# Kernel optimization log

Hardware: AMD Instinct MI355X
Metric: run time of the kernel (lower is better)

The kernel has to match this reference:

```python
import math
import jax, jax.numpy as jnp
import numpy as np

B, S, E, H = 2, 2048, 1024, 16
Dh = E // H  # 64
ROPE_BASE = 10000.0


def setup_inputs() -> dict:
    key = jax.random.key(0)
    ks = jax.random.split(key, 7)
    f32 = jnp.float32
    return {
        "q": jax.random.normal(ks[0], (B, S, E), dtype=f32),
        "k": jax.random.normal(ks[1], (B, S, E), dtype=f32),
        "v": jax.random.normal(ks[2], (B, S, E), dtype=f32),
        # nn.Linear weights stored torch-style as [out_features, in_features]
        "W_q": jax.random.normal(ks[3], (E, E), dtype=f32) * 0.02,
        "W_k": jax.random.normal(ks[4], (E, E), dtype=f32) * 0.02,
        "W_v": jax.random.normal(ks[5], (E, E), dtype=f32) * 0.02,
        "W_o": jax.random.normal(ks[6], (E, E), dtype=f32) * 0.02,
    }


def _rope(x):
    # x: [B, H, S, Dh]; interleaved-pair rotary embedding along the seq axis.
    d = x.shape[-1]
    pos = jnp.arange(x.shape[2], dtype=x.dtype)
    inv_freq = 1.0 / (ROPE_BASE ** (jnp.arange(0, d, 2, dtype=x.dtype) / d))
    ang = pos[:, None] * inv_freq            # [S, Dh//2]
    cos, sin = jnp.cos(ang), jnp.sin(ang)    # broadcast over [B, H]
    xe, xo = x[..., 0::2], x[..., 1::2]      # even/odd interleaved pairs
    out = jnp.stack([xe * cos - xo * sin, xo * cos + xe * sin], axis=-1)
    return out.reshape(x.shape)


def reference(q, k, v, W_q, W_k, W_v, W_o):
    b, s, e = q.shape
    scale = 1.0 / math.sqrt(e)  # NOTE: 1/sqrt(hidden_dim), not head_dim (faithful)
    # project and split heads: [B, H, S, Dh]
    qh = (q @ W_q.T).reshape(b, s, H, Dh).transpose(0, 2, 1, 3)
    kh = (k @ W_k.T).reshape(b, s, H, Dh).transpose(0, 2, 1, 3)
    vh = (v @ W_v.T).reshape(b, s, H, Dh).transpose(0, 2, 1, 3)
    qh = _rope(qh)
    kh = _rope(kh)
    scores = jnp.einsum('bhsd,bhtd->bhst', qh, kh) * scale
    # Faithful quirk: the original sets causal_mask[0,0] = False, which zeroes
    # the ENTIRE [S,S] mask (dims 0,1 are singletons) -> masked_fill is a no-op.
    probs = jax.nn.softmax(scores, axis=-1)
    out = jnp.einsum('bhst,bhtd->bhsd', probs, vh)
    out = out.transpose(0, 2, 1, 3).reshape(b, s, e)
    return out @ W_o.T
```

## Files before the change

kernel.cpp:

```cpp
#include <hip/hip_runtime.h>
#include <math.h>

#define Bsz 2
#define Ssz 2048
#define Esz 1024
#define Hn  16
#define Dd  64
#define PADC 72
#define TP   136
#define FP   68

typedef unsigned short ushort_t;
typedef short bf16x8 __attribute__((ext_vector_type(8)));
typedef short bf16x4 __attribute__((ext_vector_type(4)));
typedef float f32x4 __attribute__((ext_vector_type(4)));

#define GLD16(g, l) __builtin_amdgcn_global_load_lds(                        \
    (const __attribute__((address_space(1))) unsigned int*)(g),              \
    (__attribute__((address_space(3))) unsigned int*)(l), 16, 0, 0)

#define KF 0.045084220027780106f

#define MFMA32(a, b, c) __builtin_amdgcn_mfma_f32_16x16x32_bf16((a), (b), (c), 0, 0, 0)
#define MFMA16(a, b, c) __builtin_amdgcn_mfma_f32_16x16x16bf16_1k((a), (b), (c), 0, 0, 0)

__device__ inline ushort_t bf16_rn(float x)
{
    unsigned u = __float_as_uint(x);
    return (ushort_t)((u + 0x7FFFu + ((u >> 16) & 1u)) >> 16);
}

__global__ __launch_bounds__(256) void cvt_kernel(
    const float* s0, const float* s1, const float* s2, const float* s3,
    const float* s4, const float* s5, const float* s6,
    ushort_t* d0, ushort_t* d1, ushort_t* d2, ushort_t* d3,
    ushort_t* d4, ushort_t* d5, ushort_t* d6,
    float* tc, float* ts, int n_big, int n_small)
{
    if (blockIdx.z == 7) {
        const int idx = blockIdx.x * 256 + threadIdx.x;
        if (idx < Ssz * 32) {
            const int s = idx >> 5, p = idx & 31;
            const double c = 9.210340371976184257 / 32.0;
            const double inv = exp(-c * (double)p);
            double sn, cs;
            sincos((double)s * inv, &sn, &cs);
            tc[idx] = (float)cs;
            ts[idx] = (float)sn;
        }
        return;
    }
    const float* s; ushort_t* d;
    switch (blockIdx.z) {
        case 0: s = s0; d = d0; break;
        case 1: s = s1; d = d1; break;
        case 2: s = s2; d = d2; break;
        case 3: s = s3; d = d3; break;
        case 4: s = s4; d = d4; break;
        case 5: s = s5; d = d5; break;
        default: s = s6; d = d6; break;
    }
    const int n = (blockIdx.z < 3) ? n_big : n_small;
    const int i = (blockIdx.x * 256 + threadIdx.x) * 4;
    if (i >= n) return;
    float4 v = *(const float4*)(s + i);
    ushort4 o;
    o.x = bf16_rn(v.x); o.y = bf16_rn(v.y);
    o.z = bf16_rn(v.z); o.w = bf16_rn(v.w);
    *(ushort4*)(d + i) = o;
}

__global__ __launch_bounds__(256) void proj_gemm_kernel(
    const ushort_t* __restrict__ Aq, const ushort_t* __restrict__ Ak,
    const ushort_t* __restrict__ Av,
    const ushort_t* __restrict__ Wq, const ushort_t* __restrict__ Wk,
    const ushort_t* __restrict__ Wv,
    ushort_t* __restrict__ Yq, ushort_t* __restrict__ Yk,
    ushort_t* __restrict__ Yv,
    const float* __restrict__ tc, const float* __restrict__ ts)
{
    const int z = blockIdx.z;
    const ushort_t* Ag = (z == 0) ? Aq : (z == 1) ? Ak : Av;
    const ushort_t* Wg = (z == 0) ? Wq : (z == 1) ? Wk : Wv;
    ushort_t*       Yg = (z == 0) ? Yq : (z == 1) ? Yk : Yv;

    __shared__ __align__(16) char smem[128 * TP * 2];
    ushort_t* sA = (ushort_t*)smem;
    ushort_t* sB = sA + 128 * 32;
    ushort_t* Tb = (ushort_t*)smem;

    const int t    = threadIdx.x;
    const int lane = t & 63;
    const int w    = t >> 6;
    const int wm   = (w & 1) * 64;
    const int wn   = (w >> 1) * 64;
    const int fr   = lane & 15;
    const int g    = lane >> 4;
    const int kq   = g * 8;
    const int n0   = blockIdx.x * 128;
    const int m0   = blockIdx.y * 128;

    const ushort_t* pA = Ag + (size_t)(m0 + (t >> 2)) * 1024 + (t & 3) * 8;
    const ushort_t* pB = Wg + (size_t)(n0 + (t >> 2)) * 1024 + (t & 3) * 8;

    f32x4 acc[4][4];
#pragma unroll
    for (int mi = 0; mi < 4; ++mi)
#pragma unroll
        for (int ni = 0; ni < 4; ++ni) acc[mi][ni] = (f32x4)0.f;

    for (int k0 = 0; k0 < 1024; k0 += 32) {
        GLD16(pA + k0,             &sA[t * 8]);
        GLD16(pA + k0 + 64 * 1024, &sA[2048 + t * 8]);
        GLD16(pB + k0,             &sB[t * 8]);
        GLD16(pB + k0 + 64 * 1024, &sB[2048 + t * 8]);
        __syncthreads();

        bf16x8 a[4], b[4];
#pragma unroll
        for (int mi = 0; mi < 4; ++mi)
            a[mi] = *(const bf16x8*)&sA[(wm + mi * 16 + fr) * 32 + kq];
#pragma unroll
        for (int ni = 0; ni < 4; ++ni)
            b[ni] = *(const bf16x8*)&sB[(wn + ni * 16 + fr) * 32 + kq];
#pragma unroll
        for (int mi = 0; mi < 4; ++mi)
#pragma unroll
            for (int ni = 0; ni < 4; ++ni)
                acc[mi][ni] = MFMA32(a[mi], b[ni], acc[mi][ni]);
        __syncthreads();
    }

#pragma unroll
    for (int mi = 0; mi < 4; ++mi)
#pragma unroll
        for (int ni = 0; ni < 4; ++ni) {
            const int col = wn + ni * 16 + fr;
            const int d   = (n0 + col) & 63;
            const int pi  = d >> 1;
#pragma unroll
            for (int rg = 0; rg < 4; ++rg) {
                const int row = wm + mi * 16 + g * 4 + rg;
                const int s   = (m0 + row) & (Ssz - 1);
                float v  = acc[mi][ni][rg];
                float pt = __shfl_xor(v, 1, 64);
                float o  = v;
                if (z < 2) {
                    const float cs = tc[s * 32 + pi];
                    const float sn = ts[s * 32 + pi];
                    o = (d & 1) ? fmaf(v, cs, pt * sn)
                                : fmaf(v, cs, -pt * sn);
                    if (z == 0) o *= KF;
                }
                Tb[row * TP + col] = bf16_rn(o);
            }
        }
    __syncthreads();

    if (z < 2) {
        const int row = t >> 1;
        const int m   = m0 + row;
        const int b   = m >> 11, s = m & (Ssz - 1);
#pragma unroll
        for (int i = 0; i < 8; ++i) {
            const int ic = (t & 1) * 8 + i;
            uint4 val = *(const uint4*)&Tb[row * TP + ic * 8];
            const int hh = (n0 >> 6) + (ic >> 3);
            const int d  = (ic & 7) * 8;
            *(uint4*)&Yg[(((size_t)(b * Hn + hh)) * Ssz + s) * Dd + d] = val;
        }
    } else {
        const int col = t >> 1;
        const int hh  = (n0 >> 6) + (col >> 6);
        const int d   = col & 63;
        const int b   = m0 >> 11;
        const int sg  = (m0 & (Ssz - 1)) + (t & 1) * 64;
        const size_t base = (((size_t)(b * Hn + hh)) * Dd + d) * Ssz + sg;
#pragma unroll
        for (int jj = 0; jj < 8; ++jj) {
            uint4 val;
            unsigned vv[4];
#pragma unroll
            for (int qd = 0; qd < 4; ++qd) {
                const int r0 = (t & 1) * 64 + jj * 8 + qd * 2;
                const unsigned lo = Tb[(r0 + 0) * TP + col];
                const unsigned hi = Tb[(r0 + 1) * TP + col];
                vv[qd] = lo | (hi << 16);
            }
            val.x = vv[0]; val.y = vv[1]; val.z = vv[2]; val.w = vv[3];
            *(uint4*)&Yg[base + jj * 8] = val;
        }
    }
}

__global__ __launch_bounds__(256) void attn_kernel(
    const ushort_t* __restrict__ Qb, const ushort_t* __restrict__ Kb,
    const ushort_t* __restrict__ Vtb, ushort_t* __restrict__ Ob)
{
    __shared__ __align__(16) ushort_t sKV[4][64 * PADC];

    const int t    = threadIdx.x;
    const int lane = t & 63;
    const int w    = t >> 6;
    const int fr   = lane & 15;
    const int g    = lane >> 4;
    const int kq   = g * 8;
    const int bh   = blockIdx.y;
    const int q0   = blockIdx.x * 128;

    bf16x8 qa[2][2];
#pragma unroll
    for (int mt = 0; mt < 2; ++mt) {
        const size_t qbase = ((size_t)bh * Ssz + q0 + w * 32 + mt * 16 + fr) * Dd;
        qa[mt][0] = *(const bf16x8*)(Qb + qbase + kq);
        qa[mt][1] = *(const bf16x8*)(Qb + qbase + 32 + kq);
    }

    float lp[2] = {0.f, 0.f};
    f32x4 Oacc[2][4];
#pragma unroll
    for (int mt = 0; mt < 2; ++mt)
#pragma unroll
        for (int dt = 0; dt < 4; ++dt) Oacc[mt][dt] = (f32x4)0.f;

    const int srow = t >> 3;
    const int scol = (t & 7) * 8;
    const size_t kgb = (size_t)bh * Ssz * Dd;
    const size_t vgb = (size_t)bh * Dd * Ssz;

#pragma unroll
    for (int rr = 0; rr < 2; ++rr) {
        const int row = srow + rr * 32;
        *(uint4*)&sKV[0][row * PADC + scol] =
            *(const uint4*)(Kb + kgb + (size_t)row * Dd + scol);
        *(uint4*)&sKV[2][row * PADC + scol] =
            *(const uint4*)(Vtb + vgb + (size_t)row * Ssz + scol);
    }
    __syncthreads();

    int cur = 0;
    for (int kv0 = 0; kv0 < Ssz; kv0 += 64) {
        const bool more = (kv0 + 64 < Ssz);
        uint4 nk[2], nv[2];
        if (more) {
#pragma unroll
            for (int rr = 0; rr < 2; ++rr) {
                const int row = srow + rr * 32;
                nk[rr] = *(const uint4*)(Kb + kgb + (size_t)(kv0 + 64 + row) * Dd + scol);
                nv[rr] = *(const uint4*)(Vtb + vgb + (size_t)row * Ssz + kv0 + 64 + scol);
            }
        }
        const ushort_t* sK = sKV[cur];
        const ushort_t* sV = sKV[2 + cur];

        f32x4 St[2][4];
#pragma unroll
        for (int mt = 0; mt < 2; ++mt)
#pragma unroll
            for (int nt = 0; nt < 4; ++nt) St[mt][nt] = (f32x4)0.f;
#pragma unroll
        for (int ks = 0; ks < 2; ++ks)
#pragma unroll
            for (int nt = 0; nt < 4; ++nt) {
                bf16x8 kfrag = *(const bf16x8*)&sK[(nt * 16 + fr) * PADC + ks * 32 + kq];
#pragma unroll
                for (int mt = 0; mt < 2; ++mt)
                    St[mt][nt] = MFMA32(kfrag, qa[mt][ks], St[mt][nt]);
            }

        bf16x4 pf[2][4];
#pragma unroll
        for (int mt = 0; mt < 2; ++mt)
#pragma unroll
            for (int nt = 0; nt < 4; ++nt) {
                const float p0 = exp2f(St[mt][nt][0]);
                const float p1 = exp2f(St[mt][nt][1]);
                const float p2 = exp2f(St[mt][nt][2]);
                const float p3 = exp2f(St[mt][nt][3]);
                lp[mt] += (p0 + p1) + (p2 + p3);
                union { unsigned u[2]; bf16x4 s; } pk;
                pk.u[0] = (__float_as_uint(p0) >> 16) | (__float_as_uint(p1) & 0xFFFF0000u);
                pk.u[1] = (__float_as_uint(p2) >> 16) | (__float_as_uint(p3) & 0xFFFF0000u);
                pf[mt][nt] = pk.s;
            }

#pragma unroll
        for (int nt = 0; nt < 4; ++nt)
#pragma unroll
            for (int dt = 0; dt < 4; ++dt) {
                bf16x4 vfrag = *(const bf16x4*)&sV[(dt * 16 + fr) * PADC + nt * 16 + g * 4];
#pragma unroll
                for (int mt = 0; mt < 2; ++mt)
                    Oacc[mt][dt] = MFMA16(pf[mt][nt], vfrag, Oacc[mt][dt]);
            }

        if (more) {
#pragma unroll
            for (int rr = 0; rr < 2; ++rr) {
                const int row = srow + rr * 32;
                *(uint4*)&sKV[cur ^ 1][row * PADC + scol] = nk[rr];
                *(uint4*)&sKV[2 + (cur ^ 1)][row * PADC + scol] = nv[rr];
            }
            __syncthreads();
            cur ^= 1;
        }
    }

#pragma unroll
    for (int mt = 0; mt < 2; ++mt) {
        lp[mt] += __shfl_xor(lp[mt], 16, 64);
        lp[mt] += __shfl_xor(lp[mt], 32, 64);
    }

    const int b = bh >> 4, h = bh & 15;
#pragma unroll
    for (int mt = 0; mt < 2; ++mt)
#pragma unroll
        for (int rg = 0; rg < 4; ++rg) {
            const float lv  = __shfl(lp[mt], (lane & 48) + g * 4 + rg, 64);
            const float inv = 1.f / lv;
            const int s = q0 + w * 32 + mt * 16 + g * 4 + rg;
#pragma unroll
            for (int dt = 0; dt < 4; ++dt) {
                const float o = Oacc[mt][dt][rg] * inv;
                Ob[((size_t)(b * Ssz + s)) * Esz + h * Dd + dt * 16 + fr] = bf16_rn(o);
            }
        }
}

__global__ __launch_bounds__(256) void final_gemm_kernel(
    const ushort_t* __restrict__ Ag, const ushort_t* __restrict__ Bg,
    float* __restrict__ Yf)
{
    __shared__ __align__(16) char smem[128 * FP * 4];
    ushort_t* sA = (ushort_t*)smem;
    ushort_t* sB = sA + 128 * 32;
    float*    Tf = (float*)smem;

    const int t    = threadIdx.x;
    const int lane = t & 63;
    const int w    = t >> 6;
    const int wm   = (w & 1) * 64;
    const int wn   = (w >> 1) * 32;
    const int fr   = lane & 15;
    const int g    = lane >> 4;
    const int kq   = g * 8;
    const int n0   = blockIdx.x * 64;
    const int m0   = blockIdx.y * 128;

    const ushort_t* pA = Ag + (size_t)(m0 + (t >> 2)) * 1024 + (t & 3) * 8;
    const ushort_t* pB = Bg + (size_t)(n0 + (t >> 2)) * 1024 + (t & 3) * 8;

    f32x4 acc[4][2];
#pragma unroll
    for (int mi = 0; mi < 4; ++mi)
#pragma unroll
        for (int ni = 0; ni < 2; ++ni) acc[mi][ni] = (f32x4)0.f;

    for (int k0 = 0; k0 < 1024; k0 += 32) {
        GLD16(pA + k0,             &sA[t * 8]);
        GLD16(pA + k0 + 64 * 1024, &sA[2048 + t * 8]);
        GLD16(pB + k0,             &sB[t * 8]);
        __syncthreads();

        bf16x8 a[4], b[2];
#pragma unroll
        for (int mi = 0; mi < 4; ++mi)
            a[mi] = *(const bf16x8*)&sA[(wm + mi * 16 + fr) * 32 + kq];
#pragma unroll
        for (int ni = 0; ni < 2; ++ni)
            b[ni] = *(const bf16x8*)&sB[(wn + ni * 16 + fr) * 32 + kq];
#pragma unroll
        for (int mi = 0; mi < 4; ++mi)
#pragma unroll
            for (int ni = 0; ni < 2; ++ni)
                acc[mi][ni] = MFMA32(a[mi], b[ni], acc[mi][ni]);
        __syncthreads();
    }

#pragma unroll
    for (int mi = 0; mi < 4; ++mi)
#pragma unroll
        for (int ni = 0; ni < 2; ++ni) {
            const int col = wn + ni * 16 + fr;
#pragma unroll
            for (int rg = 0; rg < 4; ++rg)
                Tf[(wm + mi * 16 + g * 4 + rg) * FP + col] = acc[mi][ni][rg];
        }
    __syncthreads();

    const int row = t >> 1;
    float* dst = Yf + (size_t)(m0 + row) * 1024 + n0 + (t & 1) * 32;
    const float* src = &Tf[row * FP + (t & 1) * 32];
#pragma unroll
    for (int i = 0; i < 8; ++i)
        *(float4*)(dst + i * 4) = *(const float4*)(src + i * 4);
}

extern "C" void kernel_launch(void* const* d_in, const int* in_sizes, int n_in,
                              void* d_out, int out_size, void* d_ws, size_t ws_size,
                              hipStream_t stream)
{
    (void)in_sizes; (void)n_in; (void)out_size; (void)ws_size;
    const float* q   = (const float*)d_in[0];
    const float* k   = (const float*)d_in[1];
    const float* v   = (const float*)d_in[2];
    const float* W_q = (const float*)d_in[3];
    const float* W_k = (const float*)d_in[4];
    const float* W_v = (const float*)d_in[5];
    const float* W_o = (const float*)d_in[6];
    float* out = (float*)d_out;

    const size_t NQ = (size_t)Bsz * Ssz * Esz;
    const size_t NW = (size_t)Esz * Esz;

    float* ws = (float*)d_ws;
    float* tc = ws;
    float* ts = ws + 65536;

    ushort_t* us  = (ushort_t*)(ws + 131072);
    ushort_t* qb  = us;
    ushort_t* kb  = qb + NQ;
    ushort_t* vb  = kb + NQ;
    ushort_t* wqb = vb + NQ;
    ushort_t* wkb = wqb + NW;
    ushort_t* wvb = wkb + NW;
    ushort_t* wob = wvb + NW;
    ushort_t* pq  = wob + NW;
    ushort_t* pk  = pq + NQ;
    ushort_t* pv  = pk + NQ;
    ushort_t* ob  = pv + NQ;

    dim3 blk(256);

    cvt_kernel<<<dim3(4096, 1, 8), blk, 0, stream>>>(
        q, k, v, W_q, W_k, W_v, W_o,
        qb, kb, vb, wqb, wkb, wvb, wob, tc, ts, (int)NQ, (int)NW);

    proj_gemm_kernel<<<dim3(Esz / 128, (Bsz * Ssz) / 128, 3), blk, 0, stream>>>(
        qb, kb, vb, wqb, wkb, wvb, pq, pk, pv, tc, ts);

    attn_kernel<<<dim3(Ssz / 128, Bsz * Hn), blk, 0, stream>>>(pq, pk, pv, ob);

    final_gemm_kernel<<<dim3(Esz / 64, (Bsz * Ssz) / 128), blk, 0, stream>>>(
        ob, wob, out);
}
```

Baseline: 302.0 us.

## Load K/V tiles directly to LDS with global_load_lds and XOR-swizzled layout

Replaces the register-staged K/V prefetch (global load into registers, then store to padded LDS) with direct global-to-LDS 16-byte loads into the next buffer. Since those loads write to contiguous per-thread LDS slots, the padded row layout is replaced by an XOR swizzle of 8-element chunks by row, and the K and V fragment reads are re-indexed to match. This frees prefetch registers and removes the LDS store instructions, but it depends on the barrier correctly covering completion of the async loads.

```diff
diff --git a/kernel.cpp b/kernel.cpp
--- a/kernel.cpp
+++ b/kernel.cpp
@@ -6,7 +6,7 @@
 #define Esz 1024
 #define Hn  16
 #define Dd  64
-#define PADC 72
+#define PK   64
 #define TP   136
 #define FP   68
 
@@ -197,7 +197,7 @@
     const ushort_t* __restrict__ Qb, const ushort_t* __restrict__ Kb,
     const ushort_t* __restrict__ Vtb, ushort_t* __restrict__ Ob)
 {
-    __shared__ __align__(16) ushort_t sKV[4][64 * PADC];
+    __shared__ __align__(16) ushort_t sKV[4][64 * PK];
 
     const int t    = threadIdx.x;
     const int lane = t & 63;
@@ -223,32 +223,33 @@
 #pragma unroll
         for (int dt = 0; dt < 4; ++dt) Oacc[mt][dt] = (f32x4)0.f;
 
-    const int srow = t >> 3;
-    const int scol = (t & 7) * 8;
+    const int r1 = t >> 3;
+    const int r2 = r1 + 32;
+    const int j1 = (t & 7) ^ (r1 & 7);
     const size_t kgb = (size_t)bh * Ssz * Dd;
     const size_t vgb = (size_t)bh * Dd * Ssz;
 
-#pragma unroll
-    for (int rr = 0; rr < 2; ++rr) {
-        const int row = srow + rr * 32;
-        *(uint4*)&sKV[0][row * PADC + scol] =
-            *(const uint4*)(Kb + kgb + (size_t)row * Dd + scol);
-        *(uint4*)&sKV[2][row * PADC + scol] =
-            *(const uint4*)(Vtb + vgb + (size_t)row * Ssz + scol);
-    }
+    const int f7 = fr & 7;
+
+    GLD16(Kb  + kgb + (size_t)r1 * Dd  + j1 * 8, &sKV[0][t * 8]);
+    GLD16(Kb  + kgb + (size_t)r2 * Dd  + j1 * 8, &sKV[0][2048 + t * 8]);
+    GLD16(Vtb + vgb + (size_t)r1 * Ssz + j1 * 8, &sKV[2][t * 8]);
+    GLD16(Vtb + vgb + (size_t)r2 * Ssz + j1 * 8, &sKV[2][2048 + t * 8]);
     __syncthreads();
 
     int cur = 0;
     for (int kv0 = 0; kv0 < Ssz; kv0 += 64) {
         const bool more = (kv0 + 64 < Ssz);
-        uint4 nk[2], nv[2];
         if (more) {
-#pragma unroll
-            for (int rr = 0; rr < 2; ++rr) {
-                const int row = srow + rr * 32;
-                nk[rr] = *(const uint4*)(Kb + kgb + (size_t)(kv0 + 64 + row) * Dd + scol);
-                nv[rr] = *(const uint4*)(Vtb + vgb + (size_t)row * Ssz + kv0 + 64 + scol);
-            }
+            const int nb = cur ^ 1;
+            GLD16(Kb  + kgb + (size_t)(kv0 + 64 + r1) * Dd + j1 * 8,
+                  &sKV[nb][t * 8]);
+            GLD16(Kb  + kgb + (size_t)(kv0 + 64 + r2) * Dd + j1 * 8,
+                  &sKV[nb][2048 + t * 8]);
+            GLD16(Vtb + vgb + (size_t)r1 * Ssz + kv0 + 64 + j1 * 8,
+                  &sKV[2 + nb][t * 8]);
+            GLD16(Vtb + vgb + (size_t)r2 * Ssz + kv0 + 64 + j1 * 8,
+                  &sKV[2 + nb][2048 + t * 8]);
         }
         const ushort_t* sK = sKV[cur];
         const ushort_t* sV = sKV[2 + cur];
@@ -262,7 +263,8 @@
         for (int ks = 0; ks < 2; ++ks)
 #pragma unroll
             for (int nt = 0; nt < 4; ++nt) {
-                bf16x8 kfrag = *(const bf16x8*)&sK[(nt * 16 + fr) * PADC + ks * 32 + kq];
+                const int ch = (ks * 4 + g) ^ f7;
+                bf16x8 kfrag = *(const bf16x8*)&sK[(nt * 16 + fr) * PK + ch * 8];
 #pragma unroll
                 for (int mt = 0; mt < 2; ++mt)
                     St[mt][nt] = MFMA32(kfrag, qa[mt][ks], St[mt][nt]);
@@ -288,19 +290,15 @@
         for (int nt = 0; nt < 4; ++nt)
 #pragma unroll
             for (int dt = 0; dt < 4; ++dt) {
-                bf16x4 vfrag = *(const bf16x4*)&sV[(dt * 16 + fr) * PADC + nt * 16 + g * 4];
+                const int ch = (2 * nt + (g >> 1)) ^ f7;
+                bf16x4 vfrag = *(const bf16x4*)
+                    &sV[(dt * 16 + fr) * PK + ch * 8 + (g & 1) * 4];
 #pragma unroll
                 for (int mt = 0; mt < 2; ++mt)
                     Oacc[mt][dt] = MFMA16(pf[mt][nt], vfrag, Oacc[mt][dt]);
             }
 
         if (more) {
-#pragma unroll
-            for (int rr = 0; rr < 2; ++rr) {
-                const int row = srow + rr * 32;
-                *(uint4*)&sKV[cur ^ 1][row * PADC + scol] = nk[rr];
-                *(uint4*)&sKV[2 + (cur ^ 1)][row * PADC + scol] = nv[rr];
-            }
             __syncthreads();
             cur ^= 1;
         }
```

After: 271.7 us. 10.0% less time.
